# Kernel tuning notes

Hardware: AMD Instinct MI355X
Metric: run time of the kernel (lower is better)

Reference implementation:

```python
import jax, jax.numpy as jnp
import numpy as np

N, CIN, C, L = 6144, 6, 128, 3
SIGMA = 0.3

def _ln(x, g, b, eps=1e-5):
    m = x.mean(-1, keepdims=True)
    v = x.var(-1, keepdims=True)
    return (x - m) / jnp.sqrt(v + eps) * g + b

def _cdist(a):
    n2 = jnp.sum(a * a, -1)
    d2 = n2[:, None] + n2[None, :] - 2.0 * (a @ a.T)
    return jnp.sqrt(jnp.maximum(d2, 0.0))

def setup_inputs():
    key = jax.random.key(0)
    ks = jax.random.split(key, 24)
    s = 1.0 / np.sqrt(C)
    ref = jax.random.normal(ks[0], (N, 3), dtype=jnp.float32)
    src = ref + 0.05 * jax.random.normal(ks[1], (N, 3), dtype=jnp.float32)
    return {
        "ref_keypts": ref,
        "src_keypts": src,
        "corr_feat": jax.random.normal(ks[2], (N, CIN), dtype=jnp.float32),
        "W_in": jax.random.normal(ks[3], (CIN + 6, C), dtype=jnp.float32) * (1.0 / np.sqrt(CIN + 6)),
        "b_in": jnp.zeros((C,), jnp.float32),
        "mlp_W": jax.random.normal(ks[4], (L, C, C), dtype=jnp.float32) * s,
        "mlp_b": jnp.zeros((L, C), jnp.float32),
        "mlp_g": jnp.ones((L, C), jnp.float32),
        "mlp_beta": jnp.zeros((L, C), jnp.float32),
        "Wq": jax.random.normal(ks[5], (L, C, C), dtype=jnp.float32) * s,
        "bq": jnp.zeros((L, C), jnp.float32),
        "Wk": jax.random.normal(ks[6], (L, C, C), dtype=jnp.float32) * s,
        "bk": jnp.zeros((L, C), jnp.float32),
        "Wv": jax.random.normal(ks[7], (L, C, C), dtype=jnp.float32) * s,
        "bv": jnp.zeros((L, C), jnp.float32),
        "Wo": jax.random.normal(ks[8], (L, C, C), dtype=jnp.float32) * s,
        "bo": jnp.zeros((L, C), jnp.float32),
        "ln_g": jnp.ones((L, C), jnp.float32),
        "ln_b": jnp.zeros((L, C), jnp.float32),
        "c1_W": jax.random.normal(ks[9], (C, 32), dtype=jnp.float32) * s,
        "c1_b": jnp.zeros((32,), jnp.float32),
        "c2_W": jax.random.normal(ks[10], (32, 32), dtype=jnp.float32) * (1.0 / np.sqrt(32)),
        "c2_b": jnp.zeros((32,), jnp.float32),
        "c3_W": jax.random.normal(ks[11], (32, 1), dtype=jnp.float32) * (1.0 / np.sqrt(32)),
        "c3_b": jnp.zeros((1,), jnp.float32),
    }

def reference(ref_keypts, src_keypts, corr_feat, W_in, b_in, mlp_W, mlp_b, mlp_g, mlp_beta, Wq, bq, Wk, bk, Wv, bv, Wo, bo, ln_g, ln_b, c1_W, c1_b, c2_W, c2_b, c3_W, c3_b):
    # keypoint-diff embedding
    kp = jnp.concatenate([ref_keypts, src_keypts], -1)          # [N, 6]
    kp = kp - kp.mean(-1, keepdims=True)
    feat = jnp.concatenate([corr_feat, kp], -1) @ W_in + b_in   # [N, C]
    # geometric compatibility (no grad in original -> stop_gradient)
    geo = _cdist(ref_keypts) - _cdist(src_keypts)               # [N, N]
    geo = jnp.maximum(1.0 - geo * geo / (SIGMA * SIGMA), 0.0)
    geo = jax.lax.stop_gradient(geo)
    scale = 1.0 / np.sqrt(C)
    for i in range(L):
        # UnaryBlock: Linear -> norm -> LeakyReLU(0.1)
        h = _ln(feat @ mlp_W[i] + mlp_b[i], mlp_g[i], mlp_beta[i])
        feat = jnp.where(h > 0, h, 0.1 * h)
        # AttentionLayer (1 head) with multiplicative attention_factors
        q = feat @ Wq[i] + bq[i]
        k = feat @ Wk[i] + bk[i]
        v = feat @ Wv[i] + bv[i]
        attn = jax.nn.softmax(geo * ((q @ k.T) * scale), axis=-1)  # [N, N]
        hid = (attn @ v) @ Wo[i] + bo[i]
        feat = _ln(hid + feat, ln_g[i], ln_b[i])
    feat = feat / jnp.maximum(jnp.linalg.norm(feat, axis=-1, keepdims=True), 1e-12)
    h = jax.nn.relu(feat @ c1_W + c1_b)
    h = jax.nn.relu(h @ c2_W + c2_b)
    score = jax.nn.sigmoid(h @ c3_W + c3_b)[:, 0]
    return feat, score
```

## Files before the change

kernel.cpp:

```cpp
#include <hip/hip_runtime.h>
#include <math.h>

#define NPTS 6144
#define CH   128

typedef __attribute__((ext_vector_type(8))) short short8;
typedef __attribute__((ext_vector_type(4))) float f32x4;
typedef __attribute__((ext_vector_type(2))) float f32x2;
typedef __attribute__((ext_vector_type(4))) int   i32x4;
typedef __attribute__((ext_vector_type(2))) int   i32x2;

__device__ inline ushort f2bf(float f) {
  union { float f; unsigned u; } v; v.f = f;
  unsigned u = v.u;
  u += 0x7fff + ((u >> 16) & 1);
  return (ushort)(u >> 16);
}

__device__ inline f32x2 splat2(float x) { return (f32x2){x, x}; }

__device__ inline float fsqrt(float x) {
  float r; asm("v_sqrt_f32 %0, %1" : "=v"(r) : "v"(x)); return r;
}
__device__ inline float fexp2(float x) {
  float r; asm("v_exp_f32 %0, %1" : "=v"(r) : "v"(x)); return r;
}

__global__ __launch_bounds__(128) void k_embed(
    const float* __restrict__ refp, const float* __restrict__ srcp,
    const float* __restrict__ cf, const float* __restrict__ Win,
    const float* __restrict__ bin, float* __restrict__ out) {
  const int row = blockIdx.x, j = threadIdx.x;
  __shared__ float inb[12];
  __shared__ float mkp;
  if (j < 6)       inb[j] = cf[row * 6 + j];
  else if (j < 9)  inb[j] = refp[row * 3 + (j - 6)];
  else if (j < 12) inb[j] = srcp[row * 3 + (j - 9)];
  __syncthreads();
  if (j == 0) {
    float s = inb[6] + inb[7] + inb[8] + inb[9] + inb[10] + inb[11];
    mkp = s * (1.0f / 6.0f);
  }
  __syncthreads();
  float acc = bin[j];
  #pragma unroll
  for (int kk = 0; kk < 12; kk++) {
    float x = inb[kk] - (kk >= 6 ? mkp : 0.0f);
    acc = fmaf(x, Win[kk * CH + j], acc);
  }
  out[row * CH + j] = acc;
}

template <bool RESID, bool LEAKY>
__global__ __launch_bounds__(128) void k_row_linear_ln(
    const float* __restrict__ X, const float* __restrict__ W,
    const float* __restrict__ b, const float* __restrict__ g,
    const float* __restrict__ beta, const float* __restrict__ res,
    float* __restrict__ out) {
  const int j = threadIdx.x;
  const int r0 = blockIdx.x * 4;
  __shared__ float xs[4][CH];
  __shared__ float red[2][4];
  #pragma unroll
  for (int r = 0; r < 4; r++) xs[r][j] = X[(r0 + r) * CH + j];
  __syncthreads();

  float acc[4];
  const float bj = b[j];
  #pragma unroll
  for (int r = 0; r < 4; r++) acc[r] = bj;
  for (int kk = 0; kk < CH; kk++) {
    float w = W[kk * CH + j];
    #pragma unroll
    for (int r = 0; r < 4; r++) acc[r] = fmaf(xs[r][kk], w, acc[r]);
  }
  if (RESID) {
    #pragma unroll
    for (int r = 0; r < 4; r++) acc[r] += res[(r0 + r) * CH + j];
  }

  const int wv = j >> 6, ln = j & 63;
  float sum[4];
  #pragma unroll
  for (int r = 0; r < 4; r++) sum[r] = acc[r];
  #pragma unroll
  for (int o = 32; o; o >>= 1) {
    #pragma unroll
    for (int r = 0; r < 4; r++) sum[r] += __shfl_xor(sum[r], o);
  }
  if (ln == 0) {
    #pragma unroll
    for (int r = 0; r < 4; r++) red[wv][r] = sum[r];
  }
  __syncthreads();
  float mean[4], dv[4];
  #pragma unroll
  for (int r = 0; r < 4; r++) {
    mean[r] = (red[0][r] + red[1][r]) * (1.0f / 128.0f);
    dv[r] = acc[r] - mean[r];
    sum[r] = dv[r] * dv[r];
  }
  #pragma unroll
  for (int o = 32; o; o >>= 1) {
    #pragma unroll
    for (int r = 0; r < 4; r++) sum[r] += __shfl_xor(sum[r], o);
  }
  __syncthreads();
  if (ln == 0) {
    #pragma unroll
    for (int r = 0; r < 4; r++) red[wv][r] = sum[r];
  }
  __syncthreads();
  const float gj = g[j], betaj = beta[j];
  #pragma unroll
  for (int r = 0; r < 4; r++) {
    float var = (red[0][r] + red[1][r]) * (1.0f / 128.0f);
    float y = dv[r] * rsqrtf(var + 1e-5f) * gj + betaj;
    if (LEAKY) y = (y > 0.0f) ? y : 0.1f * y;
    out[(r0 + r) * CH + j] = y;
  }
}

__global__ __launch_bounds__(128) void k_qkv(
    const float* __restrict__ X,
    const float* __restrict__ Wq, const float* __restrict__ bq,
    const float* __restrict__ Wk, const float* __restrict__ bk,
    const float* __restrict__ Wv, const float* __restrict__ bv,
    ushort* __restrict__ Q, ushort* __restrict__ K, ushort* __restrict__ Vt) {
  const int j = threadIdx.x;
  const int r0 = blockIdx.x * 4;
  __shared__ float xs[4][CH];
  #pragma unroll
  for (int r = 0; r < 4; r++) xs[r][j] = X[(r0 + r) * CH + j];
  __syncthreads();
  float aq[4], ak[4], av[4];
  const float bqj = bq[j], bkj = bk[j], bvj = bv[j];
  #pragma unroll
  for (int r = 0; r < 4; r++) { aq[r] = bqj; ak[r] = bkj; av[r] = bvj; }
  for (int kk = 0; kk < CH; kk++) {
    float wq = Wq[kk * CH + j], wk = Wk[kk * CH + j], wv = Wv[kk * CH + j];
    #pragma unroll
    for (int r = 0; r < 4; r++) {
      float x = xs[r][kk];
      aq[r] = fmaf(x, wq, aq[r]);
      ak[r] = fmaf(x, wk, ak[r]);
      av[r] = fmaf(x, wv, av[r]);
    }
  }
  const float scale = 0.12751879524143007f;
  #pragma unroll
  for (int r = 0; r < 4; r++) {
    Q[(r0 + r) * CH + j] = f2bf(aq[r] * scale);
    K[(r0 + r) * CH + j] = f2bf(ak[r]);
  }
  ushort4 vp;
  vp.x = f2bf(av[0]); vp.y = f2bf(av[1]); vp.z = f2bf(av[2]); vp.w = f2bf(av[3]);
  *(ushort4*)(Vt + (size_t)j * NPTS + r0) = vp;
}

__global__ __launch_bounds__(256) void k_attn_mfma(
    const ushort* __restrict__ Q, const ushort* __restrict__ K,
    const ushort* __restrict__ Vt,
    const float* __restrict__ refp, const float* __restrict__ srcp,
    float* __restrict__ Opart, float* __restrict__ ML, int ntiles) {
  const int tid = threadIdx.x;
  const int w = tid >> 6, ln = tid & 63;
  const int l15 = ln & 15, g = ln >> 4;
  const int row0 = blockIdx.x * 64;
  const int seg = blockIdx.y;
  const int t0 = seg * ntiles;

  __shared__ ushort Ks[64 * 128];
  __shared__ ushort Vts[128][72];
  __shared__ float cs2[6][64];

  short8 qf[4];
  {
    const ushort* qp = Q + (size_t)(row0 + 16 * w + l15) * CH + 8 * g;
    #pragma unroll
    for (int ks = 0; ks < 4; ks++) qf[ks] = *(const short8*)(qp + 32 * ks);
  }
  const int qrow = row0 + 16 * w + l15;
  const float rq0 = refp[qrow * 3], rq1 = refp[qrow * 3 + 1], rq2 = refp[qrow * 3 + 2];
  const float sq0 = srcp[qrow * 3], sq1 = srcp[qrow * 3 + 1], sq2 = srcp[qrow * 3 + 2];

  f32x4 oacc[8];
  #pragma unroll
  for (int n = 0; n < 8; n++) oacc[n] = (f32x4){0.f, 0.f, 0.f, 0.f};
  float m = -1e30f, l = 0.0f;
  const float invs2 = 1.0f / (0.3f * 0.3f);

  for (int tt = 0; tt < ntiles; tt++) {
    const int t = t0 + tt;
    __syncthreads();
    #pragma unroll
    for (int s = 0; s < 4; s++) {
      int idx = tid + 256 * s;
      int row = idx >> 4, c8 = idx & 15;
      char* dst = (char*)Ks + row * 256 + ((c8 * 16) ^ ((row & 7) << 4));
      *(short8*)dst = *(const short8*)(K + (size_t)(t * 64 + row) * CH + c8 * 8);
    }
    #pragma unroll
    for (int s = 0; s < 4; s++) {
      int idx = tid + 256 * s;
      int c = idx >> 3, j8 = idx & 7;
      *(short8*)&Vts[c][j8 * 8] =
          *(const short8*)(Vt + (size_t)c * NPTS + t * 64 + j8 * 8);
    }
    if (tid < 64) {
      int gj = t * 64 + tid;
      cs2[0][tid] = refp[gj * 3];     cs2[1][tid] = refp[gj * 3 + 1];
      cs2[2][tid] = refp[gj * 3 + 2]; cs2[3][tid] = srcp[gj * 3];
      cs2[4][tid] = srcp[gj * 3 + 1]; cs2[5][tid] = srcp[gj * 3 + 2];
    }
    __syncthreads();

    f32x4 acc[4];
    #pragma unroll
    for (int nb = 0; nb < 4; nb++) acc[nb] = (f32x4){0.f, 0.f, 0.f, 0.f};
    __builtin_amdgcn_s_setprio(1);
    #pragma unroll
    for (int ks = 0; ks < 4; ks++) {
      #pragma unroll
      for (int nb = 0; nb < 4; nb++) {
        int krow = 16 * nb + l15;
        const char* src = (const char*)Ks + krow * 256 +
                          ((64 * ks + 16 * g) ^ ((krow & 7) << 4));
        short8 af = *(const short8*)src;
        acc[nb] = __builtin_amdgcn_mfma_f32_16x16x32_bf16(af, qf[ks], acc[nb], 0, 0, 0);
      }
    }
    __builtin_amdgcn_s_setprio(0);

    float plog[4][4];
    #pragma unroll
    for (int nb = 0; nb < 4; nb++) {
      const int kb = 16 * nb + 4 * g;
      #pragma unroll
      for (int pp = 0; pp < 2; pp++) {
        const int k2 = kb + 2 * pp;
        f32x2 cx = *(const f32x2*)&cs2[0][k2];
        f32x2 cy = *(const f32x2*)&cs2[1][k2];
        f32x2 cz = *(const f32x2*)&cs2[2][k2];
        f32x2 dx = splat2(rq0) - cx, dy = splat2(rq1) - cy, dz = splat2(rq2) - cz;
        f32x2 d2r = dx * dx + dy * dy + dz * dz;
        cx = *(const f32x2*)&cs2[3][k2];
        cy = *(const f32x2*)&cs2[4][k2];
        cz = *(const f32x2*)&cs2[5][k2];
        dx = splat2(sq0) - cx; dy = splat2(sq1) - cy; dz = splat2(sq2) - cz;
        f32x2 d2s = dx * dx + dy * dy + dz * dz;
        f32x2 prod = d2r * d2s;
        f32x2 sum2 = d2r + d2s;
        float s0 = fsqrt(prod[0]), s1 = fsqrt(prod[1]);
        float dd20 = fmaf(-2.0f, s0, sum2[0]);
        float dd21 = fmaf(-2.0f, s1, sum2[1]);
        float gg0 = fmaxf(fmaf(dd20, -invs2, 1.0f), 0.0f);
        float gg1 = fmaxf(fmaf(dd21, -invs2, 1.0f), 0.0f);
        plog[nb][2 * pp]     = gg0 * acc[nb][2 * pp];
        plog[nb][2 * pp + 1] = gg1 * acc[nb][2 * pp + 1];
      }
    }

    float tm = fmaxf(fmaxf(plog[0][0], plog[0][1]), fmaxf(plog[0][2], plog[0][3]));
    #pragma unroll
    for (int nb = 1; nb < 4; nb++) {
      float t2 = fmaxf(fmaxf(plog[nb][0], plog[nb][1]),
                       fmaxf(plog[nb][2], plog[nb][3]));
      tm = fmaxf(tm, t2);
    }
    tm = fmaxf(tm, __shfl_xor(tm, 16));
    tm = fmaxf(tm, __shfl_xor(tm, 32));
    if (__any(tm > m + 11.0f)) {
      float nm = fmaxf(m, tm);
      float rsc = fexp2(m - nm);
      l *= rsc;
      #pragma unroll
      for (int n = 0; n < 8; n++) oacc[n] *= rsc;
      m = nm;
    }
    float psum = 0.0f;
    #pragma unroll
    for (int nb = 0; nb < 4; nb++)
      #pragma unroll
      for (int r = 0; r < 4; r++) {
        float p = fexp2(plog[nb][r] - m);
        plog[nb][r] = p;
        psum += p;
      }
    psum += __shfl_xor(psum, 16);
    psum += __shfl_xor(psum, 32);
    l += psum;

    unsigned pk[4][2];
    #pragma unroll
    for (int nb = 0; nb < 4; nb++) {
      asm("v_cvt_pk_bf16_f32 %0, %1, %2"
          : "=v"(pk[nb][0]) : "v"(plog[nb][0]), "v"(plog[nb][1]));
      asm("v_cvt_pk_bf16_f32 %0, %1, %2"
          : "=v"(pk[nb][1]) : "v"(plog[nb][2]), "v"(plog[nb][3]));
    }

    union U16 { i32x4 i; short8 s; };
    __builtin_amdgcn_s_setprio(1);
    #pragma unroll
    for (int ks2 = 0; ks2 < 2; ks2++) {
      U16 b;
      b.i[0] = (int)pk[2 * ks2][0];
      b.i[1] = (int)pk[2 * ks2][1];
      b.i[2] = (int)pk[2 * ks2 + 1][0];
      b.i[3] = (int)pk[2 * ks2 + 1][1];
      #pragma unroll
      for (int nb2 = 0; nb2 < 8; nb2++) {
        const ushort* vp2 = &Vts[16 * nb2 + l15][32 * ks2 + 4 * g];
        i32x2 a0 = *(const i32x2*)vp2;
        i32x2 a1 = *(const i32x2*)(vp2 + 16);
        U16 a;
        a.i[0] = a0[0]; a.i[1] = a0[1]; a.i[2] = a1[0]; a.i[3] = a1[1];
        oacc[nb2] = __builtin_amdgcn_mfma_f32_16x16x32_bf16(a.s, b.s, oacc[nb2], 0, 0, 0);
      }
    }
    __builtin_amdgcn_s_setprio(0);
  }

  {
    float* op = Opart + ((size_t)seg * NPTS + qrow) * CH;
    #pragma unroll
    for (int nb2 = 0; nb2 < 8; nb2++)
      *(f32x4*)(op + 16 * nb2 + 4 * g) = oacc[nb2];
    if (g == 0) {
      ML[((size_t)seg * NPTS + qrow) * 2]     = m;
      ML[((size_t)seg * NPTS + qrow) * 2 + 1] = l;
    }
  }
}

__global__ __launch_bounds__(256) void k_attn_combine(
    const float* __restrict__ Opart, const float* __restrict__ ML,
    float* __restrict__ out, int NS) {
  const int tid = threadIdx.x;
  const int row = blockIdx.x * 8 + (tid >> 5);
  const int c4 = (tid & 31) * 4;
  float M = -1e30f;
  for (int s = 0; s < NS; s++)
    M = fmaxf(M, ML[((size_t)s * NPTS + row) * 2]);
  float L = 0.0f;
  f32x4 acc = (f32x4){0.f, 0.f, 0.f, 0.f};
  for (int s = 0; s < NS; s++) {
    float ms = ML[((size_t)s * NPTS + row) * 2];
    float ls = ML[((size_t)s * NPTS + row) * 2 + 1];
    float wsc = fexp2(ms - M);
    L += wsc * ls;
    f32x4 o = *(const f32x4*)&Opart[((size_t)s * NPTS + row) * CH + c4];
    acc[0] = fmaf(wsc, o[0], acc[0]);
    acc[1] = fmaf(wsc, o[1], acc[1]);
    acc[2] = fmaf(wsc, o[2], acc[2]);
    acc[3] = fmaf(wsc, o[3], acc[3]);
  }
  float inv = 1.0f / L;
  f32x4 r = acc * (f32x4){inv, inv, inv, inv};
  *(f32x4*)&out[(size_t)row * CH + c4] = r;
}

__global__ __launch_bounds__(128) void k_final(
    const float* __restrict__ F,
    const float* __restrict__ c1W, const float* __restrict__ c1b,
    const float* __restrict__ c2W, const float* __restrict__ c2b,
    const float* __restrict__ c3W, const float* __restrict__ c3b,
    float* __restrict__ out) {
  const int row = blockIdx.x, j = threadIdx.x;
  __shared__ float xs[CH];
  __shared__ float h1[32];
  __shared__ float h2[32];
  __shared__ float red[2];
  float x = F[row * CH + j];
  float ss = x * x;
  #pragma unroll
  for (int o = 32; o; o >>= 1) ss += __shfl_xor(ss, o);
  if ((j & 63) == 0) red[j >> 6] = ss;
  __syncthreads();
  float norm = sqrtf(red[0] + red[1]);
  float xn = x / fmaxf(norm, 1e-12f);
  xs[j] = xn;
  out[row * CH + j] = xn;
  __syncthreads();
  if (j < 32) {
    float a = c1b[j];
    for (int kk = 0; kk < CH; kk++) a = fmaf(xs[kk], c1W[kk * 32 + j], a);
    h1[j] = fmaxf(a, 0.0f);
  }
  __syncthreads();
  if (j < 32) {
    float a = c2b[j];
    #pragma unroll
    for (int kk = 0; kk < 32; kk++) a = fmaf(h1[kk], c2W[kk * 32 + j], a);
    h2[j] = fmaxf(a, 0.0f);
  }
  __syncthreads();
  if (j == 0) {
    float a = c3b[0];
    #pragma unroll
    for (int kk = 0; kk < 32; kk++) a = fmaf(h2[kk], c3W[kk], a);
    out[NPTS * CH + row] = 1.0f / (1.0f + __expf(-a));
  }
}

extern "C" void kernel_launch(void* const* d_in, const int* in_sizes, int n_in,
                              void* d_out, int out_size, void* d_ws, size_t ws_size,
                              hipStream_t stream) {
  const float* refp = (const float*)d_in[0];
  const float* srcp = (const float*)d_in[1];
  const float* cf   = (const float*)d_in[2];
  const float* Win  = (const float*)d_in[3];
  const float* bin  = (const float*)d_in[4];
  const float* mlpW = (const float*)d_in[5];
  const float* mlpb = (const float*)d_in[6];
  const float* mlpg = (const float*)d_in[7];
  const float* mlpbeta = (const float*)d_in[8];
  const float* Wq = (const float*)d_in[9];
  const float* bq = (const float*)d_in[10];
  const float* Wk = (const float*)d_in[11];
  const float* bk = (const float*)d_in[12];
  const float* Wv = (const float*)d_in[13];
  const float* bv = (const float*)d_in[14];
  const float* Wo = (const float*)d_in[15];
  const float* bo = (const float*)d_in[16];
  const float* lng = (const float*)d_in[17];
  const float* lnb = (const float*)d_in[18];
  const float* c1W = (const float*)d_in[19];
  const float* c1b = (const float*)d_in[20];
  const float* c2W = (const float*)d_in[21];
  const float* c2b = (const float*)d_in[22];
  const float* c3W = (const float*)d_in[23];
  const float* c3b = (const float*)d_in[24];
  float* out = (float*)d_out;

  const size_t NC = (size_t)NPTS * CH;
  float* F = (float*)d_ws;
  float* T = F + NC;
  float* A = T + NC;
  ushort* Qb  = (ushort*)(A + NC);
  ushort* Kb  = Qb + NC;
  ushort* Vtb = Kb + NC;
  float* Opart = (float*)(Vtb + NC);

  const size_t base_bytes = 3 * NC * 4 + 3 * NC * 2;
  int NS = 1;
  for (int cand = 16; cand >= 2; cand >>= 1) {
    size_t need = base_bytes + (size_t)cand * (NC * 4 + NPTS * 8);
    if (need <= ws_size) { NS = cand; break; }
  }
  float* ML = Opart + (size_t)NS * NC;
  const int ntiles = NPTS / 64 / NS;

  k_embed<<<NPTS, 128, 0, stream>>>(refp, srcp, cf, Win, bin, F);
  for (int i = 0; i < 3; i++) {
    const int o2 = i * CH * CH, o1 = i * CH;
    k_row_linear_ln<false, true><<<NPTS / 4, 128, 0, stream>>>(
        F, mlpW + o2, mlpb + o1, mlpg + o1, mlpbeta + o1, nullptr, T);
    k_qkv<<<NPTS / 4, 128, 0, stream>>>(
        T, Wq + o2, bq + o1, Wk + o2, bk + o1, Wv + o2, bv + o1, Qb, Kb, Vtb);
    dim3 agrid(NPTS / 64, NS);
    k_attn_mfma<<<agrid, 256, 0, stream>>>(Qb, Kb, Vtb, refp, srcp, Opart, ML, ntiles);
    k_attn_combine<<<NPTS / 8, 256, 0, stream>>>(Opart, ML, A, NS);
    k_row_linear_ln<true, false><<<NPTS / 4, 128, 0, stream>>>(
        A, Wo + o2, bo + o1, lng + o1, lnb + o1, T, F);
  }
  k_final<<<NPTS, 128, 0, stream>>>(F, c1W, c1b, c2W, c2b, c3W, c3b, out);
}
```

Baseline: 372.2 us.

## Fuse MLP+QKV and combine+out-proj, pipeline attention with async LDS loads

The MLP linear+LN+LeakyReLU kernel is merged with the QKV projection, and the split-softmax combine is merged with the output projection+residual+LN. This removes two launches per layer and the round trip through global memory. The attention kernel now runs 512 threads over 128 query rows per block. It double-buffers K tiles using global_load_lds direct-to-LDS loads and prefetches coordinates, and stores V in a permuted, XOR-swizzled layout so each MFMA operand is one 16-byte read. The trade-offs are more LDS per block, more complex synchronisation, and combine work now done with less parallelism inside k_out.

```diff
diff --git a/kernel.cpp b/kernel.cpp
--- a/kernel.cpp
+++ b/kernel.cpp
@@ -8,7 +8,6 @@
 typedef __attribute__((ext_vector_type(4))) float f32x4;
 typedef __attribute__((ext_vector_type(2))) float f32x2;
 typedef __attribute__((ext_vector_type(4))) int   i32x4;
-typedef __attribute__((ext_vector_type(2))) int   i32x2;
 
 __device__ inline ushort f2bf(float f) {
   union { float f; unsigned u; } v; v.f = f;
@@ -24,6 +23,12 @@
 }
 __device__ inline float fexp2(float x) {
   float r; asm("v_exp_f32 %0, %1" : "=v"(r) : "v"(x)); return r;
+}
+
+__device__ inline void gload16(const void* g, void* l) {
+  __builtin_amdgcn_global_load_lds(
+      (const __attribute__((address_space(1))) unsigned int*)g,
+      (__attribute__((address_space(3))) unsigned int*)l, 16, 0, 0);
 }
 
 __global__ __launch_bounds__(128) void k_embed(
@@ -51,15 +56,19 @@
   out[row * CH + j] = acc;
 }
 
-template <bool RESID, bool LEAKY>
-__global__ __launch_bounds__(128) void k_row_linear_ln(
+__global__ __launch_bounds__(128) void k_mlp_qkv(
     const float* __restrict__ X, const float* __restrict__ W,
     const float* __restrict__ b, const float* __restrict__ g,
-    const float* __restrict__ beta, const float* __restrict__ res,
-    float* __restrict__ out) {
+    const float* __restrict__ beta,
+    const float* __restrict__ Wq, const float* __restrict__ bq,
+    const float* __restrict__ Wk, const float* __restrict__ bk,
+    const float* __restrict__ Wv, const float* __restrict__ bv,
+    float* __restrict__ T, ushort* __restrict__ Q, ushort* __restrict__ K,
+    ushort* __restrict__ Vt) {
   const int j = threadIdx.x;
   const int r0 = blockIdx.x * 4;
   __shared__ float xs[4][CH];
+  __shared__ float hs[4][CH];
   __shared__ float red[2][4];
   #pragma unroll
   for (int r = 0; r < 4; r++) xs[r][j] = X[(r0 + r) * CH + j];
@@ -70,16 +79,11 @@
   #pragma unroll
   for (int r = 0; r < 4; r++) acc[r] = bj;
   for (int kk = 0; kk < CH; kk++) {
-    float w = W[kk * CH + j];
-    #pragma unroll
-    for (int r = 0; r < 4; r++) acc[r] = fmaf(xs[r][kk], w, acc[r]);
-  }
-  if (RESID) {
-    #pragma unroll
-    for (int r = 0; r < 4; r++) acc[r] += res[(r0 + r) * CH + j];
-  }
-
-  const int wv = j >> 6, ln = j & 63;
+    float wv_ = W[kk * CH + j];
+    #pragma unroll
+    for (int r = 0; r < 4; r++) acc[r] = fmaf(xs[r][kk], wv_, acc[r]);
+  }
+  const int wv2 = j >> 6, ln = j & 63;
   float sum[4];
   #pragma unroll
   for (int r = 0; r < 4; r++) sum[r] = acc[r];
@@ -90,14 +94,14 @@
   }
   if (ln == 0) {
     #pragma unroll
-    for (int r = 0; r < 4; r++) red[wv][r] = sum[r];
-  }
-  __syncthreads();
-  float mean[4], dv[4];
+    for (int r = 0; r < 4; r++) red[wv2][r] = sum[r];
+  }
+  __syncthreads();
+  float dv[4];
   #pragma unroll
   for (int r = 0; r < 4; r++) {
-    mean[r] = (red[0][r] + red[1][r]) * (1.0f / 128.0f);
-    dv[r] = acc[r] - mean[r];
+    float mean = (red[0][r] + red[1][r]) * (1.0f / 128.0f);
+    dv[r] = acc[r] - mean;
     sum[r] = dv[r] * dv[r];
   }
   #pragma unroll
@@ -108,7 +112,7 @@
   __syncthreads();
   if (ln == 0) {
     #pragma unroll
-    for (int r = 0; r < 4; r++) red[wv][r] = sum[r];
+    for (int r = 0; r < 4; r++) red[wv2][r] = sum[r];
   }
   __syncthreads();
   const float gj = g[j], betaj = beta[j];
@@ -116,35 +120,24 @@
   for (int r = 0; r < 4; r++) {
     float var = (red[0][r] + red[1][r]) * (1.0f / 128.0f);
     float y = dv[r] * rsqrtf(var + 1e-5f) * gj + betaj;
-    if (LEAKY) y = (y > 0.0f) ? y : 0.1f * y;
-    out[(r0 + r) * CH + j] = y;
-  }
-}
-
-__global__ __launch_bounds__(128) void k_qkv(
-    const float* __restrict__ X,
-    const float* __restrict__ Wq, const float* __restrict__ bq,
-    const float* __restrict__ Wk, const float* __restrict__ bk,
-    const float* __restrict__ Wv, const float* __restrict__ bv,
-    ushort* __restrict__ Q, ushort* __restrict__ K, ushort* __restrict__ Vt) {
-  const int j = threadIdx.x;
-  const int r0 = blockIdx.x * 4;
-  __shared__ float xs[4][CH];
-  #pragma unroll
-  for (int r = 0; r < 4; r++) xs[r][j] = X[(r0 + r) * CH + j];
-  __syncthreads();
+    y = (y > 0.0f) ? y : 0.1f * y;
+    T[(r0 + r) * CH + j] = y;
+    hs[r][j] = y;
+  }
+  __syncthreads();
+
   float aq[4], ak[4], av[4];
   const float bqj = bq[j], bkj = bk[j], bvj = bv[j];
   #pragma unroll
   for (int r = 0; r < 4; r++) { aq[r] = bqj; ak[r] = bkj; av[r] = bvj; }
   for (int kk = 0; kk < CH; kk++) {
-    float wq = Wq[kk * CH + j], wk = Wk[kk * CH + j], wv = Wv[kk * CH + j];
+    float wq = Wq[kk * CH + j], wk = Wk[kk * CH + j], wv_ = Wv[kk * CH + j];
     #pragma unroll
     for (int r = 0; r < 4; r++) {
-      float x = xs[r][kk];
+      float x = hs[r][kk];
       aq[r] = fmaf(x, wq, aq[r]);
       ak[r] = fmaf(x, wk, ak[r]);
-      av[r] = fmaf(x, wv, av[r]);
+      av[r] = fmaf(x, wv_, av[r]);
     }
   }
   const float scale = 0.12751879524143007f;
@@ -155,10 +148,13 @@
   }
   ushort4 vp;
   vp.x = f2bf(av[0]); vp.y = f2bf(av[1]); vp.z = f2bf(av[2]); vp.w = f2bf(av[3]);
-  *(ushort4*)(Vt + (size_t)j * NPTS + r0) = vp;
-}
-
-__global__ __launch_bounds__(256) void k_attn_mfma(
+  const int w0 = r0 & 63;
+  const int pos = (r0 & ~63) + 32 * ((w0 >> 5) & 1) + 8 * ((w0 >> 2) & 3) +
+                  4 * ((w0 >> 4) & 1);
+  *(ushort4*)(Vt + (size_t)j * NPTS + pos) = vp;
+}
+
+__global__ __launch_bounds__(512, 6) void k_attn_mfma(
     const ushort* __restrict__ Q, const ushort* __restrict__ K,
     const ushort* __restrict__ Vt,
     const float* __restrict__ refp, const float* __restrict__ srcp,
@@ -166,13 +162,28 @@
   const int tid = threadIdx.x;
   const int w = tid >> 6, ln = tid & 63;
   const int l15 = ln & 15, g = ln >> 4;
-  const int row0 = blockIdx.x * 64;
+  const int row0 = blockIdx.x * 128;
   const int seg = blockIdx.y;
   const int t0 = seg * ntiles;
 
-  __shared__ ushort Ks[64 * 128];
-  __shared__ ushort Vts[128][72];
+  __shared__ ushort Ks[2][64][128];
+  __shared__ ushort Vs[128][64];
   __shared__ float cs2[6][64];
+
+  const int krow = tid >> 4;
+  const int ksc  = ((tid & 15) ^ (krow & 7)) * 8;
+  const int vch  = tid >> 3;
+  const int vsc  = ((tid & 7) ^ (vch & 7)) * 8;
+  char* kdst = (char*)&Ks[0][0][0] + (tid & ~63) * 16;
+  char* vdst = (char*)&Vs[0][0] + (tid & ~63) * 16;
+
+  float cr[6];
+
+  f32x4 oacc[8];
+  #pragma unroll
+  for (int n = 0; n < 8; n++) oacc[n] = (f32x4){0.f, 0.f, 0.f, 0.f};
+  float m = -1e30f, l = 0.0f;
+  const float invs2 = 1.0f / (0.3f * 0.3f);
 
   short8 qf[4];
   {
@@ -184,36 +195,47 @@
   const float rq0 = refp[qrow * 3], rq1 = refp[qrow * 3 + 1], rq2 = refp[qrow * 3 + 2];
   const float sq0 = srcp[qrow * 3], sq1 = srcp[qrow * 3 + 1], sq2 = srcp[qrow * 3 + 2];
 
-  f32x4 oacc[8];
-  #pragma unroll
-  for (int n = 0; n < 8; n++) oacc[n] = (f32x4){0.f, 0.f, 0.f, 0.f};
-  float m = -1e30f, l = 0.0f;
-  const float invs2 = 1.0f / (0.3f * 0.3f);
-
+  if (tid < 64) {
+    int gj = t0 * 64 + tid;
+    cr[0] = refp[gj * 3]; cr[1] = refp[gj * 3 + 1]; cr[2] = refp[gj * 3 + 2];
+    cr[3] = srcp[gj * 3]; cr[4] = srcp[gj * 3 + 1]; cr[5] = srcp[gj * 3 + 2];
+  }
+  {
+    const ushort* s0 = K + (size_t)(t0 * 64 + krow) * CH + ksc;
+    const ushort* s1 = K + (size_t)(t0 * 64 + krow + 32) * CH + ksc;
+    gload16(s0, kdst);
+    gload16(s1, kdst + 8192);
+    const ushort* v0 = Vt + (size_t)vch * NPTS + t0 * 64 + vsc;
+    const ushort* v1 = Vt + (size_t)(vch + 64) * NPTS + t0 * 64 + vsc;
+    gload16(v0, vdst);
+    gload16(v1, vdst + 8192);
+    if (ntiles > 1) {
+      const ushort* s2 = K + (size_t)((t0 + 1) * 64 + krow) * CH + ksc;
+      const ushort* s3 = K + (size_t)((t0 + 1) * 64 + krow + 32) * CH + ksc;
+      gload16(s2, kdst + 16384);
+      gload16(s3, kdst + 16384 + 8192);
+    }
+  }
+  if (tid < 64) {
+    #pragma unroll
+    for (int d = 0; d < 6; d++) cs2[d][tid] = cr[d];
+  }
+  __syncthreads();
+
+  int cb = 0;
   for (int tt = 0; tt < ntiles; tt++) {
     const int t = t0 + tt;
-    __syncthreads();
-    #pragma unroll
-    for (int s = 0; s < 4; s++) {
-      int idx = tid + 256 * s;
-      int row = idx >> 4, c8 = idx & 15;
-      char* dst = (char*)Ks + row * 256 + ((c8 * 16) ^ ((row & 7) << 4));
-      *(short8*)dst = *(const short8*)(K + (size_t)(t * 64 + row) * CH + c8 * 8);
-    }
-    #pragma unroll
-    for (int s = 0; s < 4; s++) {
-      int idx = tid + 256 * s;
-      int c = idx >> 3, j8 = idx & 7;
-      *(short8*)&Vts[c][j8 * 8] =
-          *(const short8*)(Vt + (size_t)c * NPTS + t * 64 + j8 * 8);
-    }
-    if (tid < 64) {
-      int gj = t * 64 + tid;
-      cs2[0][tid] = refp[gj * 3];     cs2[1][tid] = refp[gj * 3 + 1];
-      cs2[2][tid] = refp[gj * 3 + 2]; cs2[3][tid] = srcp[gj * 3];
-      cs2[4][tid] = srcp[gj * 3 + 1]; cs2[5][tid] = srcp[gj * 3 + 2];
-    }
-    __syncthreads();
+    if (tt > 0) {
+      const ushort* v0 = Vt + (size_t)vch * NPTS + t * 64 + vsc;
+      const ushort* v1 = Vt + (size_t)(vch + 64) * NPTS + t * 64 + vsc;
+      gload16(v0, vdst);
+      gload16(v1, vdst + 8192);
+    }
+    if (tt + 1 < ntiles && tid < 64) {
+      int gj = (t + 1) * 64 + tid;
+      cr[0] = refp[gj * 3]; cr[1] = refp[gj * 3 + 1]; cr[2] = refp[gj * 3 + 2];
+      cr[3] = srcp[gj * 3]; cr[4] = srcp[gj * 3 + 1]; cr[5] = srcp[gj * 3 + 2];
+    }
 
     f32x4 acc[4];
     #pragma unroll
@@ -223,9 +245,8 @@
     for (int ks = 0; ks < 4; ks++) {
       #pragma unroll
       for (int nb = 0; nb < 4; nb++) {
-        int krow = 16 * nb + l15;
-        const char* src = (const char*)Ks + krow * 256 +
-                          ((64 * ks + 16 * g) ^ ((krow & 7) << 4));
+        const char* src = (const char*)&Ks[cb][0][0] + (16 * nb + l15) * 256 +
+                          ((64 * ks + 16 * g) ^ ((l15 & 7) << 4));
         short8 af = *(const short8*)src;
         acc[nb] = __builtin_amdgcn_mfma_f32_16x16x32_bf16(af, qf[ks], acc[nb], 0, 0, 0);
       }
@@ -300,26 +321,41 @@
           : "=v"(pk[nb][1]) : "v"(plog[nb][2]), "v"(plog[nb][3]));
     }
 
+    __syncthreads();
+
+    if (tt + 2 < ntiles) {
+      const ushort* s0 = K + (size_t)((t + 2) * 64 + krow) * CH + ksc;
+      const ushort* s1 = K + (size_t)((t + 2) * 64 + krow + 32) * CH + ksc;
+      char* d = kdst + cb * 16384;
+      gload16(s0, d);
+      gload16(s1, d + 8192);
+    }
+
     union U16 { i32x4 i; short8 s; };
     __builtin_amdgcn_s_setprio(1);
     #pragma unroll
     for (int ks2 = 0; ks2 < 2; ks2++) {
-      U16 b;
-      b.i[0] = (int)pk[2 * ks2][0];
-      b.i[1] = (int)pk[2 * ks2][1];
-      b.i[2] = (int)pk[2 * ks2 + 1][0];
-      b.i[3] = (int)pk[2 * ks2 + 1][1];
+      U16 bfr;
+      bfr.i[0] = (int)pk[2 * ks2][0];
+      bfr.i[1] = (int)pk[2 * ks2][1];
+      bfr.i[2] = (int)pk[2 * ks2 + 1][0];
+      bfr.i[3] = (int)pk[2 * ks2 + 1][1];
       #pragma unroll
       for (int nb2 = 0; nb2 < 8; nb2++) {
-        const ushort* vp2 = &Vts[16 * nb2 + l15][32 * ks2 + 4 * g];
-        i32x2 a0 = *(const i32x2*)vp2;
-        i32x2 a1 = *(const i32x2*)(vp2 + 16);
-        U16 a;
-        a.i[0] = a0[0]; a.i[1] = a0[1]; a.i[2] = a1[0]; a.i[3] = a1[1];
-        oacc[nb2] = __builtin_amdgcn_mfma_f32_16x16x32_bf16(a.s, b.s, oacc[nb2], 0, 0, 0);
+        const char* vsrc = (const char*)&Vs[0][0] + (16 * nb2 + l15) * 128 +
+                           (((4 * ks2 + g) ^ (l15 & 7)) << 4);
+        short8 vf = *(const short8*)vsrc;
+        oacc[nb2] = __builtin_amdgcn_mfma_f32_16x16x32_bf16(vf, bfr.s, oacc[nb2], 0, 0, 0);
       }
     }
     __builtin_amdgcn_s_setprio(0);
+
+    if (tt + 1 < ntiles && tid < 64) {
+      #pragma unroll
+      for (int d = 0; d < 6; d++) cs2[d][tid] = cr[d];
+    }
+    __syncthreads();
+    cb ^= 1;
   }
 
   {
@@ -334,31 +370,84 @@
   }
 }
 
-__global__ __launch_bounds__(256) void k_attn_combine(
-    const float* __restrict__ Opart, const float* __restrict__ ML,
-    float* __restrict__ out, int NS) {
-  const int tid = threadIdx.x;
-  const int row = blockIdx.x * 8 + (tid >> 5);
-  const int c4 = (tid & 31) * 4;
-  float M = -1e30f;
-  for (int s = 0; s < NS; s++)
-    M = fmaxf(M, ML[((size_t)s * NPTS + row) * 2]);
-  float L = 0.0f;
-  f32x4 acc = (f32x4){0.f, 0.f, 0.f, 0.f};
-  for (int s = 0; s < NS; s++) {
-    float ms = ML[((size_t)s * NPTS + row) * 2];
-    float ls = ML[((size_t)s * NPTS + row) * 2 + 1];
-    float wsc = fexp2(ms - M);
-    L += wsc * ls;
-    f32x4 o = *(const f32x4*)&Opart[((size_t)s * NPTS + row) * CH + c4];
-    acc[0] = fmaf(wsc, o[0], acc[0]);
-    acc[1] = fmaf(wsc, o[1], acc[1]);
-    acc[2] = fmaf(wsc, o[2], acc[2]);
-    acc[3] = fmaf(wsc, o[3], acc[3]);
-  }
-  float inv = 1.0f / L;
-  f32x4 r = acc * (f32x4){inv, inv, inv, inv};
-  *(f32x4*)&out[(size_t)row * CH + c4] = r;
+__global__ __launch_bounds__(128) void k_out(
+    const float* __restrict__ Opart, const float* __restrict__ ML, int NS,
+    const float* __restrict__ W, const float* __restrict__ b,
+    const float* __restrict__ g, const float* __restrict__ beta,
+    const float* __restrict__ res, float* __restrict__ out) {
+  const int j = threadIdx.x;
+  const int r0 = blockIdx.x * 4;
+  __shared__ float xs[4][CH];
+  __shared__ float red[2][4];
+
+  #pragma unroll
+  for (int r = 0; r < 4; r++) {
+    const int row = r0 + r;
+    float M = -1e30f;
+    for (int s = 0; s < NS; s++)
+      M = fmaxf(M, ML[((size_t)s * NPTS + row) * 2]);
+    float L = 0.0f, a = 0.0f;
+    for (int s = 0; s < NS; s++) {
+      float ms = ML[((size_t)s * NPTS + row) * 2];
+      float ls = ML[((size_t)s * NPTS + row) * 2 + 1];
+      float wsc = fexp2(ms - M);
+      L += wsc * ls;
+      a = fmaf(wsc, Opart[((size_t)s * NPTS + row) * CH + j], a);
+    }
+    xs[r][j] = a / L;
+  }
+  __syncthreads();
+
+  float acc[4];
+  const float bj = b[j];
+  #pragma unroll
+  for (int r = 0; r < 4; r++) acc[r] = bj;
+  for (int kk = 0; kk < CH; kk++) {
+    float wv_ = W[kk * CH + j];
+    #pragma unroll
+    for (int r = 0; r < 4; r++) acc[r] = fmaf(xs[r][kk], wv_, acc[r]);
+  }
+  #pragma unroll
+  for (int r = 0; r < 4; r++) acc[r] += res[(r0 + r) * CH + j];
+
+  const int wv2 = j >> 6, ln = j & 63;
+  float sum[4];
+  #pragma unroll
+  for (int r = 0; r < 4; r++) sum[r] = acc[r];
+  #pragma unroll
+  for (int o = 32; o; o >>= 1) {
+    #pragma unroll
+    for (int r = 0; r < 4; r++) sum[r] += __shfl_xor(sum[r], o);
+  }
+  if (ln == 0) {
+    #pragma unroll
+    for (int r = 0; r < 4; r++) red[wv2][r] = sum[r];
+  }
+  __syncthreads();
+  float dv[4];
+  #pragma unroll
+  for (int r = 0; r < 4; r++) {
+    float mean = (red[0][r] + red[1][r]) * (1.0f / 128.0f);
+    dv[r] = acc[r] - mean;
+    sum[r] = dv[r] * dv[r];
+  }
+  #pragma unroll
+  for (int o = 32; o; o >>= 1) {
+    #pragma unroll
+    for (int r = 0; r < 4; r++) sum[r] += __shfl_xor(sum[r], o);
+  }
+  __syncthreads();
+  if (ln == 0) {
+    #pragma unroll
+    for (int r = 0; r < 4; r++) red[wv2][r] = sum[r];
+  }
+  __syncthreads();
+  const float gj = g[j], betaj = beta[j];
+  #pragma unroll
+  for (int r = 0; r < 4; r++) {
+    float var = (red[0][r] + red[1][r]) * (1.0f / 128.0f);
+    out[(r0 + r) * CH + j] = dv[r] * rsqrtf(var + 1e-5f) * gj + betaj;
+  }
 }
 
 __global__ __launch_bounds__(128) void k_final(
@@ -437,13 +526,12 @@
   const size_t NC = (size_t)NPTS * CH;
   float* F = (float*)d_ws;
   float* T = F + NC;
-  float* A = T + NC;
-  ushort* Qb  = (ushort*)(A + NC);
+  ushort* Qb  = (ushort*)(T + NC);
   ushort* Kb  = Qb + NC;
   ushort* Vtb = Kb + NC;
   float* Opart = (float*)(Vtb + NC);
 
-  const size_t base_bytes = 3 * NC * 4 + 3 * NC * 2;
+  const size_t base_bytes = 2 * NC * 4 + 3 * NC * 2;
   int NS = 1;
   for (int cand = 16; cand >= 2; cand >>= 1) {
     size_t need = base_bytes + (size_t)cand * (NC * 4 + NPTS * 8);
@@ -455,15 +543,14 @@
   k_embed<<<NPTS, 128, 0, stream>>>(refp, srcp, cf, Win, bin, F);
   for (int i = 0; i < 3; i++) {
     const int o2 = i * CH * CH, o1 = i * CH;
-    k_row_linear_ln<false, true><<<NPTS / 4, 128, 0, stream>>>(
-        F, mlpW + o2, mlpb + o1, mlpg + o1, mlpbeta + o1, nullptr, T);
-    k_qkv<<<NPTS / 4, 128, 0, stream>>>(
-        T, Wq + o2, bq + o1, Wk + o2, bk + o1, Wv + o2, bv + o1, Qb, Kb, Vtb);
-    dim3 agrid(NPTS / 64, NS);
-    k_attn_mfma<<<agrid, 256, 0, stream>>>(Qb, Kb, Vtb, refp, srcp, Opart, ML, ntiles);
-    k_attn_combine<<<NPTS / 8, 256, 0, stream>>>(Opart, ML, A, NS);
-    k_row_linear_ln<true, false><<<NPTS / 4, 128, 0, stream>>>(
-        A, Wo + o2, bo + o1, lng + o1, lnb + o1, T, F);
+    k_mlp_qkv<<<NPTS / 4, 128, 0, stream>>>(
+        F, mlpW + o2, mlpb + o1, mlpg + o1, mlpbeta + o1,
+        Wq + o2, bq + o1, Wk + o2, bk + o1, Wv + o2, bv + o1,
+        T, Qb, Kb, Vtb);
+    dim3 agrid(NPTS / 128, NS);
+    k_attn_mfma<<<agrid, 512, 0, stream>>>(Qb, Kb, Vtb, refp, srcp, Opart, ML, ntiles);
+    k_out<<<NPTS / 4, 128, 0, stream>>>(Opart, ML, NS, Wo + o2, bo + o1,
+                                        lng + o1, lnb + o1, T, F);
   }
   k_final<<<NPTS, 128, 0, stream>>>(F, c1W, c1b, c2W, c2b, c3W, c3b, out);
 }
```

New measurement: 495.0 us. +33.0%, slower.
